# Optimization experiments

Measured on AMD Instinct MI355X. Metric: run time of the kernel, lower is better.

Reference implementation:

```python
import jax, jax.numpy as jnp
import numpy as np

B, N, D_IN, D, H = 4, 256, 600, 600, 256  # batch, nodes, in_dim, mem_dim, attn hidden


def setup_inputs() -> dict:
    key = jax.random.key(0)
    ks = jax.random.split(key, 12)
    feature = jax.random.normal(ks[0], (B, N, D_IN), dtype=jnp.float32)
    latent_adj = jax.random.randint(ks[1], (B, N, N), 0, 2).astype(jnp.float32)
    s_in = 1.0 / np.sqrt(D_IN)
    s_d = 1.0 / np.sqrt(D)
    s_2d = 1.0 / np.sqrt(2 * D)
    s_h = 1.0 / np.sqrt(H)
    W0 = jax.random.uniform(ks[2], (D_IN, D), jnp.float32, -s_in, s_in)
    b0 = jax.random.uniform(ks[3], (D,), jnp.float32, -s_in, s_in)
    W1 = jax.random.uniform(ks[4], (D, D), jnp.float32, -s_d, s_d)
    b1 = jax.random.uniform(ks[5], (D,), jnp.float32, -s_d, s_d)
    aW1 = jax.random.uniform(ks[6], (2 * D, H), jnp.float32, -s_2d, s_2d)
    ab1 = jax.random.uniform(ks[7], (H,), jnp.float32, -s_2d, s_2d)
    aW2 = jax.random.uniform(ks[8], (H,), jnp.float32, -s_h, s_h)
    ab2 = jax.random.uniform(ks[9], (1,), jnp.float32, -s_h, s_h)
    return {"feature": feature, "latent_adj": latent_adj, "W0": W0, "b0": b0,
            "W1": W1, "b1": b1, "aW1": aW1, "ab1": ab1, "aW2": aW2, "ab2": ab2}


def _gat_layer(x, Wl, bl, aW1, ab1, aW2, ab2, adj):
    h = jnp.einsum('bni,io->bno', x, Wl) + bl                    # [B,N,D]
    # Decompose first attn linear: [h_i, h_j] @ aW1 = h_i @ aW1[:D] + h_j @ aW1[D:]
    left = jnp.einsum('bnd,dh->bnh', h, aW1[:h.shape[-1]])        # i-part
    right = jnp.einsum('bnd,dh->bnh', h, aW1[h.shape[-1]:])       # j-part
    hid = jax.nn.relu(left[:, :, None, :] + right[:, None, :, :] + ab1)  # [B,N,N,H]
    e = jax.nn.leaky_relu(jnp.einsum('bijh,h->bij', hid, aW2) + ab2[0],
                          negative_slope=0.01)                    # [B,N,N]
    e = jnp.where(adj == 0, jnp.float32(-1e9), e)
    attention = jax.nn.softmax(e, axis=-1) * adj
    return jax.nn.relu(jnp.einsum('bij,bjd->bid', attention, h))


def reference(feature, latent_adj, W0, b0, W1, b1, aW1, ab1, aW2, ab2):
    h = _gat_layer(feature, W0, b0, aW1, ab1, aW2, ab2, latent_adj)
    h = _gat_layer(h, W1, b1, aW1, ab1, aW2, ab2, latent_adj)
    return h
```

## Files before the change

### kernel.cpp

```cpp
#include <hip/hip_runtime.h>
#include <hip/hip_bf16.h>

#define BATCH 4
#define NN    256
#define DD    600
#define HH    256
#define MROWS (BATCH*NN)
#define KPAD  640

typedef __attribute__((ext_vector_type(8))) short bf16x8;
typedef __attribute__((ext_vector_type(4))) float f32x4;

__device__ __forceinline__ void gload16(const void* g, void* l)
{
    __builtin_amdgcn_global_load_lds(
        (const __attribute__((address_space(1))) void*)g,
        (__attribute__((address_space(3))) void*)l, 16, 0, 0);
}

__device__ __forceinline__ void waitcnt_vm(int n)
{
    switch (n) {
    case 0:  asm volatile("s_waitcnt vmcnt(0)"  ::: "memory"); break;
    case 3:  asm volatile("s_waitcnt vmcnt(3)"  ::: "memory"); break;
    case 6:  asm volatile("s_waitcnt vmcnt(6)"  ::: "memory"); break;
    default: asm volatile("s_waitcnt vmcnt(0)"  ::: "memory"); break;
    }
}

__device__ __forceinline__ int xcd_remap(int lin, int nwg)
{
    const int q = nwg >> 3, r = nwg & 7;
    const int xcd = lin & 7, off = lin >> 3;
    return (xcd < r ? xcd * (q + 1) : r * (q + 1) + (xcd - r) * q) + off;
}

template<bool BIAS, bool RELU, bool WF32, bool WB16, bool WHT, int NK>
__global__ __launch_bounds__(256) void gemm_mfma(
    const __hip_bfloat16* __restrict__ A, const __hip_bfloat16* __restrict__ BT,
    const float* __restrict__ bias,
    float* __restrict__ Cf, __hip_bfloat16* __restrict__ Cb,
    __hip_bfloat16* __restrict__ hT,
    int lda, int ldb, int ldcf, int ldcb, int Nvalid, int biasN,
    long long sA, long long sBT, long long sCf, long long sCb)
{
    __shared__ __align__(16) char lds[49152];

    const int nwg = gridDim.x * gridDim.y * gridDim.z;
    int lin = xcd_remap(blockIdx.x + gridDim.x * (blockIdx.y + gridDim.y * blockIdx.z), nwg);
    const int bx = lin % gridDim.x;
    const int by = (lin / gridDim.x) % gridDim.y;
    const int bz = lin / (gridDim.x * gridDim.y);

    const int tid  = threadIdx.x;
    const int lane = tid & 63;
    const int wid  = tid >> 6;
    const int wr   = wid >> 1;
    const int wc   = wid & 1;
    const int row0 = by * 64;
    const int col0 = bx * 32;

    const char* Ab = (const char*)A + (bz * sA + (long long)row0 * lda) * 2;
    const char* Bb = (const char*)BT + (bz * sBT + (long long)col0 * ldb) * 2;

    const int sr   = tid >> 3;
    const int scb  = (tid & 7) * 16;
    const int scbs = scb ^ ((sr & 7) << 4);

    const char* gA0 = Ab + (long long)sr        * (lda * 2) + scbs;
    const char* gA1 = Ab + (long long)(sr + 32) * (lda * 2) + scbs;
    const char* gB0 = Bb + (long long)sr        * (ldb * 2) + scbs;

    f32x4 acc[2] = {};
    const int fr = lane & 15;
    const int kg = (lane >> 4) * 16;
    const int xv = (fr & 7) << 4;

    auto issue = [&](int t) {
        char* bA = lds + (t & 3) * 8192;
        char* bB = lds + 32768 + (t & 3) * 4096;
        const long long off = (long long)t * 128;
        gload16(gA0 + off, bA + wid * 1024);
        gload16(gA1 + off, bA + 4096 + wid * 1024);
        gload16(gB0 + off, bB + wid * 1024);
    };

    constexpr int PRE = (NK < 3) ? NK : 3;
    #pragma unroll
    for (int p = 0; p < PRE; ++p) issue(p);

    #pragma unroll
    for (int t = 0; t < NK; ++t) {
        const int imax = (t + 2 < NK - 1) ? t + 2 : NK - 1;
        waitcnt_vm(3 * (imax - t));
        __builtin_amdgcn_s_barrier();
        const char* lA = lds + (t & 3) * 8192;
        const char* lB = lds + 32768 + (t & 3) * 4096;
        #pragma unroll
        for (int ks = 0; ks < 2; ++ks) {
            const int kb = ks * 64 + kg;
            bf16x8 a0 = *(const bf16x8*)(lA + (wr * 32 + fr)      * 128 + (kb ^ xv));
            bf16x8 a1 = *(const bf16x8*)(lA + (wr * 32 + 16 + fr) * 128 + (kb ^ xv));
            bf16x8 b0 = *(const bf16x8*)(lB + (wc * 16 + fr)      * 128 + (kb ^ xv));
            acc[0] = __builtin_amdgcn_mfma_f32_16x16x32_bf16(a0, b0, acc[0], 0, 0, 0);
            acc[1] = __builtin_amdgcn_mfma_f32_16x16x32_bf16(a1, b0, acc[1], 0, 0, 0);
        }
        if (t + 3 < NK) issue(t + 3);
    }
    __syncthreads();

    const int er = (lane >> 4) * 4;
    const int ec = lane & 15;
    __hip_bfloat16* sT = (__hip_bfloat16*)lds;

    #pragma unroll
    for (int mi = 0; mi < 2; ++mi) {
        const int lr0 = wr * 32 + mi * 16 + er;
        const int lc  = wc * 16 + ec;
        const int gr = row0 + lr0;
        const int gc = col0 + lc;
        const float bv = (BIAS && gc < biasN) ? bias[gc] : 0.f;
        #pragma unroll
        for (int r = 0; r < 4; ++r) {
            float v = acc[mi][r] + bv;
            if (RELU) v = fmaxf(v, 0.f);
            const __hip_bfloat16 hv = __float2bfloat16(v);
            const long long row = gr + r;
            if (WF32 && gc < Nvalid)
                Cf[bz * sCf + row * ldcf + gc] = v;
            if (WB16)
                Cb[bz * sCb + row * ldcb + gc] = hv;
            if (WHT)
                sT[(lr0 + r) * 40 + lc] = hv;
        }
    }

    if (WHT) {
        __syncthreads();
        const int b  = row0 >> 8;
        const int i0 = row0 & 255;
        const int cc = tid >> 3;
        const int ch = tid & 7;
        const int d = col0 + cc;
        __align__(16) __hip_bfloat16 tmp[8];
        #pragma unroll
        for (int u = 0; u < 8; ++u)
            tmp[u] = sT[(ch * 8 + u) * 40 + cc];
        *(float4*)&hT[((long long)b * KPAD + d) * NN + i0 + ch * 8] = *(float4*)tmp;
    }
}

__global__ __launch_bounds__(256) void prep_kernel(
    const float* __restrict__ feature, const float* __restrict__ W0,
    const float* __restrict__ W1, const float* __restrict__ aW1,
    __hip_bfloat16* __restrict__ xb, __hip_bfloat16* __restrict__ W0T,
    __hip_bfloat16* __restrict__ W1T, __hip_bfloat16* __restrict__ aW1T)
{
    const int bid = blockIdx.x;
    const int tid = threadIdx.x;
    if (bid < 640) {
        const int idx = (bid * 256 + tid) * 4;
        const int r = idx / KPAD, c = idx % KPAD;
        float4 v = make_float4(0.f, 0.f, 0.f, 0.f);
        if (c < DD) v = *(const float4*)&feature[r * DD + c];
        __align__(8) __hip_bfloat16 o[4] = {
            __float2bfloat16(v.x), __float2bfloat16(v.y),
            __float2bfloat16(v.z), __float2bfloat16(v.w)};
        *(float2*)&xb[idx] = *(float2*)o;
        return;
    }
    __shared__ float tile[32][33];
    const int t = bid - 640;
    const int which = (t < 400) ? 0 : (t < 800) ? 1 : 2;
    const int tt = (which == 0) ? t : (which == 1) ? t - 400 : t - 800;
    const int n0 = (tt / 20) * 32;
    const int k0 = (tt % 20) * 32;
    const int tx = tid & 31, ty = tid >> 5;
    #pragma unroll
    for (int r = 0; r < 4; ++r) {
        const int k = k0 + ty + r * 8;
        const int n = n0 + tx;
        float v = 0.f;
        if (which == 0)      { if (k < DD && n < DD) v = W0[k * DD + n]; }
        else if (which == 1) { if (k < DD && n < DD) v = W1[k * DD + n]; }
        else                 { if (k < DD) v = (n < HH) ? aW1[k * HH + n]
                                                        : aW1[(DD + k) * HH + (n - HH)]; }
        tile[ty + r * 8][tx] = v;
    }
    __syncthreads();
    __hip_bfloat16* dst = (which == 0) ? W0T : (which == 1) ? W1T : aW1T;
    #pragma unroll
    for (int r = 0; r < 4; ++r) {
        const int n = n0 + ty + r * 8;
        const int k = k0 + tx;
        dst[n * KPAD + k] = __float2bfloat16(tile[tx][ty + r * 8]);
    }
}

__device__ __forceinline__ void block_max4(float* v, float (*red)[4])
{
    #pragma unroll
    for (int o = 32; o > 0; o >>= 1)
        #pragma unroll
        for (int q = 0; q < 4; ++q) v[q] = fmaxf(v[q], __shfl_down(v[q], o));
    const int lane = threadIdx.x & 63, w = threadIdx.x >> 6;
    if (lane == 0) { red[w][0]=v[0]; red[w][1]=v[1]; red[w][2]=v[2]; red[w][3]=v[3]; }
    __syncthreads();
    #pragma unroll
    for (int q = 0; q < 4; ++q)
        v[q] = fmaxf(fmaxf(red[0][q], red[1][q]), fmaxf(red[2][q], red[3][q]));
    __syncthreads();
}

__device__ __forceinline__ void block_sum4(float* v, float (*red)[4])
{
    #pragma unroll
    for (int o = 32; o > 0; o >>= 1)
        #pragma unroll
        for (int q = 0; q < 4; ++q) v[q] += __shfl_down(v[q], o);
    const int lane = threadIdx.x & 63, w = threadIdx.x >> 6;
    if (lane == 0) { red[w][0]=v[0]; red[w][1]=v[1]; red[w][2]=v[2]; red[w][3]=v[3]; }
    __syncthreads();
    #pragma unroll
    for (int q = 0; q < 4; ++q)
        v[q] = red[0][q] + red[1][q] + red[2][q] + red[3][q];
    __syncthreads();
}

__global__ __launch_bounds__(256) void attn_kernel(
    const float* __restrict__ LR, const float* __restrict__ aW2,
    const float* __restrict__ ab2, const float* __restrict__ adj,
    __hip_bfloat16* __restrict__ att)
{
    __shared__ float sL[4][HH];
    __shared__ float sW[HH];
    __shared__ float red[4][4];

    const int b  = blockIdx.y;
    const int i0 = blockIdx.x * 4;
    const int j  = threadIdx.x;

    float a[4];
    #pragma unroll
    for (int q = 0; q < 4; ++q)
        a[q] = adj[((long long)(b * NN + i0 + q)) * NN + j];
    const float ab2v = ab2[0];

    sW[j] = aW2[j];
    #pragma unroll
    for (int q = 0; q < 4; ++q)
        sL[q][j] = LR[((long long)(b * NN + i0 + q)) * 512 + j];
    __syncthreads();

    const float* rp = LR + ((long long)(b * NN + j)) * 512 + HH;
    float acc[4] = {0.f, 0.f, 0.f, 0.f};
    for (int h = 0; h < HH; h += 8) {
        const float4 ra = *(const float4*)(rp + h);
        const float4 rb = *(const float4*)(rp + h + 4);
        const float4 w0 = *(const float4*)&sW[h];
        const float4 w1 = *(const float4*)&sW[h + 4];
        #pragma unroll
        for (int q = 0; q < 4; ++q) {
            const float4 l0 = *(const float4*)&sL[q][h];
            const float4 l1 = *(const float4*)&sL[q][h + 4];
            float s = fmaxf(l0.x + ra.x, 0.f) * w0.x;
            s += fmaxf(l0.y + ra.y, 0.f) * w0.y;
            s += fmaxf(l0.z + ra.z, 0.f) * w0.z;
            s += fmaxf(l0.w + ra.w, 0.f) * w0.w;
            s += fmaxf(l1.x + rb.x, 0.f) * w1.x;
            s += fmaxf(l1.y + rb.y, 0.f) * w1.y;
            s += fmaxf(l1.z + rb.z, 0.f) * w1.z;
            s += fmaxf(l1.w + rb.w, 0.f) * w1.w;
            acc[q] += s;
        }
    }

    float m[4];
    #pragma unroll
    for (int q = 0; q < 4; ++q) {
        float e = acc[q] + ab2v;
        e = (e > 0.f) ? e : 0.01f * e;
        m[q] = (a[q] == 0.f) ? -1e9f : e;
    }
    float mx[4] = {m[0], m[1], m[2], m[3]};
    block_max4(mx, red);
    float p[4];
    #pragma unroll
    for (int q = 0; q < 4; ++q) p[q] = __expf(m[q] - mx[q]);
    float s[4] = {p[0], p[1], p[2], p[3]};
    block_sum4(s, red);
    #pragma unroll
    for (int q = 0; q < 4; ++q)
        att[((long long)(b * NN + i0 + q)) * NN + j] = __float2bfloat16(p[q] / s[q] * a[q]);
}

extern "C" void kernel_launch(void* const* d_in, const int* in_sizes, int n_in,
                              void* d_out, int out_size, void* d_ws, size_t ws_size,
                              hipStream_t stream)
{
    const float* feature = (const float*)d_in[0];
    const float* adj     = (const float*)d_in[1];
    const float* W0      = (const float*)d_in[2];
    const float* b0      = (const float*)d_in[3];
    const float* W1      = (const float*)d_in[4];
    const float* b1      = (const float*)d_in[5];
    const float* aW1     = (const float*)d_in[6];
    const float* ab1     = (const float*)d_in[7];
    const float* aW2     = (const float*)d_in[8];
    const float* ab2     = (const float*)d_in[9];
    float* out = (float*)d_out;

    __hip_bfloat16* bw = (__hip_bfloat16*)d_ws;
    __hip_bfloat16* xb   = bw;
    __hip_bfloat16* W0T  = xb   + MROWS * KPAD;
    __hip_bfloat16* W1T  = W0T  + KPAD * KPAD;
    __hip_bfloat16* aW1T = W1T  + KPAD * KPAD;
    __hip_bfloat16* hb   = aW1T + 512 * KPAD;
    __hip_bfloat16* hT   = hb   + MROWS * KPAD;
    __hip_bfloat16* att  = hT   + BATCH * KPAD * NN;
    float* LR = (float*)(att + BATCH * NN * NN);

    prep_kernel<<<1760, 256, 0, stream>>>(feature, W0, W1, aW1, xb, W0T, W1T, aW1T);

    for (int layer = 0; layer < 2; ++layer) {
        const __hip_bfloat16* WT = layer ? W1T : W0T;
        const float* bb          = layer ? b1 : b0;

        gemm_mfma<true, false, false, true, true, KPAD/64>
            <<<dim3(KPAD / 32, MROWS / 64, 1), 256, 0, stream>>>(
            xb, WT, bb, nullptr, hb, hT,
            KPAD, KPAD, 0, KPAD, 0, DD, 0, 0, 0, 0);

        gemm_mfma<true, false, true, false, false, KPAD/64>
            <<<dim3(512 / 32, MROWS / 64, 1), 256, 0, stream>>>(
            hb, aW1T, ab1, LR, nullptr, nullptr,
            KPAD, KPAD, 512, 0, 512, HH, 0, 0, 0, 0);

        attn_kernel<<<dim3(NN / 4, BATCH), 256, 0, stream>>>(LR, aW2, ab2, adj, att);

        if (layer == 0) {
            gemm_mfma<false, true, false, true, false, NN/64>
                <<<dim3(KPAD / 32, NN / 64, BATCH), 256, 0, stream>>>(
                att, hT, nullptr, nullptr, xb, nullptr,
                NN, NN, 0, KPAD, 0, 0,
                (long long)NN * NN, (long long)KPAD * NN, 0, (long long)NN * KPAD);
        } else {
            gemm_mfma<false, true, true, false, false, NN/64>
                <<<dim3(KPAD / 32, NN / 64, BATCH), 256, 0, stream>>>(
                att, hT, nullptr, out, nullptr, nullptr,
                NN, NN, DD, 0, DD, 0,
                (long long)NN * NN, (long long)KPAD * NN, (long long)NN * DD, 0);
        }
    }
}
```

Before: 64.61 us.

## Fuse attention softmax with attention-times-h GEMM in one kernel

Merges the attention-score/softmax kernel with the following attention@h batched GEMM. Each block now computes 4 attention rows, keeps them in LDS as bf16, and streams the full hT for its batch through a triple-buffered LDS pipeline into MFMA with relu applied in the epilogue. This removes one launch per layer and the global round trip of the attention matrix. In exchange, each block re-reads all of hT (256x640) for only 4 output rows. It also uses a 16-row MFMA tile where only 4 rows are valid, so most of the matrix-core work is wasted.

```diff
diff --git a/kernel.cpp b/kernel.cpp
--- a/kernel.cpp
+++ b/kernel.cpp
@@ -7,6 +7,7 @@
 #define HH    256
 #define MROWS (BATCH*NN)
 #define KPAD  640
+#define ATTS  272
 
 typedef __attribute__((ext_vector_type(8))) short bf16x8;
 typedef __attribute__((ext_vector_type(4))) float f32x4;
@@ -23,6 +24,7 @@
     switch (n) {
     case 0:  asm volatile("s_waitcnt vmcnt(0)"  ::: "memory"); break;
     case 3:  asm volatile("s_waitcnt vmcnt(3)"  ::: "memory"); break;
+    case 4:  asm volatile("s_waitcnt vmcnt(4)"  ::: "memory"); break;
     case 6:  asm volatile("s_waitcnt vmcnt(6)"  ::: "memory"); break;
     default: asm volatile("s_waitcnt vmcnt(0)"  ::: "memory"); break;
     }
@@ -35,22 +37,20 @@
     return (xcd < r ? xcd * (q + 1) : r * (q + 1) + (xcd - r) * q) + off;
 }
 
-template<bool BIAS, bool RELU, bool WF32, bool WB16, bool WHT, int NK>
+template<bool BIAS, bool WF32, bool WB16, bool WHT, int NK>
 __global__ __launch_bounds__(256) void gemm_mfma(
     const __hip_bfloat16* __restrict__ A, const __hip_bfloat16* __restrict__ BT,
     const float* __restrict__ bias,
     float* __restrict__ Cf, __hip_bfloat16* __restrict__ Cb,
     __hip_bfloat16* __restrict__ hT,
-    int lda, int ldb, int ldcf, int ldcb, int Nvalid, int biasN,
-    long long sA, long long sBT, long long sCf, long long sCb)
+    int lda, int ldb, int ldcf, int ldcb, int Nvalid, int biasN)
 {
     __shared__ __align__(16) char lds[49152];
 
-    const int nwg = gridDim.x * gridDim.y * gridDim.z;
-    int lin = xcd_remap(blockIdx.x + gridDim.x * (blockIdx.y + gridDim.y * blockIdx.z), nwg);
+    const int nwg = gridDim.x * gridDim.y;
+    int lin = xcd_remap(blockIdx.x + gridDim.x * blockIdx.y, nwg);
     const int bx = lin % gridDim.x;
-    const int by = (lin / gridDim.x) % gridDim.y;
-    const int bz = lin / (gridDim.x * gridDim.y);
+    const int by = lin / gridDim.x;
 
     const int tid  = threadIdx.x;
     const int lane = tid & 63;
@@ -60,8 +60,8 @@
     const int row0 = by * 64;
     const int col0 = bx * 32;
 
-    const char* Ab = (const char*)A + (bz * sA + (long long)row0 * lda) * 2;
-    const char* Bb = (const char*)BT + (bz * sBT + (long long)col0 * ldb) * 2;
+    const char* Ab = (const char*)A + ((long long)row0 * lda) * 2;
+    const char* Bb = (const char*)BT + ((long long)col0 * ldb) * 2;
 
     const int sr   = tid >> 3;
     const int scb  = (tid & 7) * 16;
@@ -123,13 +123,12 @@
         #pragma unroll
         for (int r = 0; r < 4; ++r) {
             float v = acc[mi][r] + bv;
-            if (RELU) v = fmaxf(v, 0.f);
             const __hip_bfloat16 hv = __float2bfloat16(v);
             const long long row = gr + r;
             if (WF32 && gc < Nvalid)
-                Cf[bz * sCf + row * ldcf + gc] = v;
+                Cf[row * ldcf + gc] = v;
             if (WB16)
-                Cb[bz * sCb + row * ldcb + gc] = hv;
+                Cb[row * ldcb + gc] = hv;
             if (WHT)
                 sT[(lr0 + r) * 40 + lc] = hv;
         }
@@ -227,18 +226,25 @@
     __syncthreads();
 }
 
-__global__ __launch_bounds__(256) void attn_kernel(
+template<bool OUTF32>
+__global__ __launch_bounds__(256) void attn_pv(
     const float* __restrict__ LR, const float* __restrict__ aW2,
     const float* __restrict__ ab2, const float* __restrict__ adj,
-    __hip_bfloat16* __restrict__ att)
-{
-    __shared__ float sL[4][HH];
-    __shared__ float sW[HH];
-    __shared__ float red[4][4];
+    const __hip_bfloat16* __restrict__ hT,
+    __hip_bfloat16* __restrict__ Ob, float* __restrict__ Of)
+{
+    __shared__ __align__(16) char smem[57344];
+    float (*sL)[HH] = (float(*)[HH])(smem + 49152);
+    float* sW       = (float*)(smem + 49152 + 4096);
+    float (*red)[4] = (float(*)[4])(smem + 49152 + 5120);
+    __hip_bfloat16* attl = (__hip_bfloat16*)(smem + 49152 + 5120 + 64);
 
     const int b  = blockIdx.y;
     const int i0 = blockIdx.x * 4;
     const int j  = threadIdx.x;
+    const int tid  = threadIdx.x;
+    const int lane = tid & 63;
+    const int wid  = tid >> 6;
 
     float a[4];
     #pragma unroll
@@ -253,7 +259,7 @@
     __syncthreads();
 
     const float* rp = LR + ((long long)(b * NN + j)) * 512 + HH;
-    float acc[4] = {0.f, 0.f, 0.f, 0.f};
+    float acs[4] = {0.f, 0.f, 0.f, 0.f};
     for (int h = 0; h < HH; h += 8) {
         const float4 ra = *(const float4*)(rp + h);
         const float4 rb = *(const float4*)(rp + h + 4);
@@ -271,14 +277,14 @@
             s += fmaxf(l1.y + rb.y, 0.f) * w1.y;
             s += fmaxf(l1.z + rb.z, 0.f) * w1.z;
             s += fmaxf(l1.w + rb.w, 0.f) * w1.w;
-            acc[q] += s;
+            acs[q] += s;
         }
     }
 
     float m[4];
     #pragma unroll
     for (int q = 0; q < 4; ++q) {
-        float e = acc[q] + ab2v;
+        float e = acs[q] + ab2v;
         e = (e > 0.f) ? e : 0.01f * e;
         m[q] = (a[q] == 0.f) ? -1e9f : e;
     }
@@ -287,11 +293,76 @@
     float p[4];
     #pragma unroll
     for (int q = 0; q < 4; ++q) p[q] = __expf(m[q] - mx[q]);
-    float s[4] = {p[0], p[1], p[2], p[3]};
-    block_sum4(s, red);
+    float s4[4] = {p[0], p[1], p[2], p[3]};
+    block_sum4(s4, red);
+
     #pragma unroll
     for (int q = 0; q < 4; ++q)
-        att[((long long)(b * NN + i0 + q)) * NN + j] = __float2bfloat16(p[q] / s[q] * a[q]);
+        attl[q * ATTS + j] = __float2bfloat16(p[q] / s4[q] * a[q]);
+
+    asm volatile("s_waitcnt lgkmcnt(0)" ::: "memory");
+    asm volatile("s_waitcnt vmcnt(0)" ::: "memory");
+    __builtin_amdgcn_s_barrier();
+
+    const char* hTb = (const char*)(hT + (long long)b * KPAD * NN);
+    const int rsub = wid * 4 + (lane >> 4);
+    const int cb16 = (lane & 15) * 16;
+
+    auto stage = [&](int c) {
+        char* buf = smem + (c % 3) * 16384;
+        const int d0 = (c >> 1) * 64;
+        const int ko = (c & 1) * 256;
+        #pragma unroll
+        for (int i = 0; i < 4; ++i) {
+            const int r = i * 16 + rsub;
+            gload16(hTb + (long long)(d0 + r) * 512 + ko + (cb16 ^ ((r & 7) << 4)),
+                    buf + i * 4096 + wid * 1024);
+        }
+    };
+
+    f32x4 acc[10] = {};
+    const int fr = lane & 15;
+    const int kg = (lane >> 4) * 16;
+    const int xv = (fr & 7) << 4;
+    const int arow = lane & 15;
+
+    stage(0); stage(1);
+    #pragma unroll
+    for (int c = 0; c < 20; ++c) {
+        waitcnt_vm(c < 19 ? 4 : 0);
+        __builtin_amdgcn_s_barrier();
+        const char* buf = smem + (c % 3) * 16384;
+        const int t  = c >> 1;
+        const int kt = c & 1;
+        #pragma unroll
+        for (int ks = 0; ks < 4; ++ks) {
+            const int kb = ks * 64 + kg;
+            bf16x8 bfr = *(const bf16x8*)(buf + (wid * 16 + fr) * 256 + (kb ^ xv));
+            bf16x8 afr = {};
+            if (arow < 4)
+                afr = *(const bf16x8*)((const char*)attl + arow * (ATTS * 2)
+                                       + (kt * 128 + ks * 32 + (lane >> 4) * 8) * 2);
+            acc[t] = __builtin_amdgcn_mfma_f32_16x16x32_bf16(afr, bfr, acc[t], 0, 0, 0);
+        }
+        if (c + 2 < 20) stage(c + 2);
+    }
+
+    if ((lane >> 4) == 0) {
+        #pragma unroll
+        for (int t = 0; t < 10; ++t) {
+            const int gc = t * 64 + wid * 16 + (lane & 15);
+            #pragma unroll
+            for (int r = 0; r < 4; ++r) {
+                const float v = fmaxf(acc[t][r], 0.f);
+                const long long row = (long long)(b * NN + i0 + r);
+                if (OUTF32) {
+                    if (gc < DD) Of[row * DD + gc] = v;
+                } else {
+                    Ob[row * KPAD + gc] = __float2bfloat16(v);
+                }
+            }
+        }
+    }
 }
 
 extern "C" void kernel_launch(void* const* d_in, const int* in_sizes, int n_in,
@@ -317,8 +388,7 @@
     __hip_bfloat16* aW1T = W1T  + KPAD * KPAD;
     __hip_bfloat16* hb   = aW1T + 512 * KPAD;
     __hip_bfloat16* hT   = hb   + MROWS * KPAD;
-    __hip_bfloat16* att  = hT   + BATCH * KPAD * NN;
-    float* LR = (float*)(att + BATCH * NN * NN);
+    float* LR = (float*)(hT + BATCH * KPAD * NN);
 
     prep_kernel<<<1760, 256, 0, stream>>>(feature, W0, W1, aW1, xb, W0T, W1T, aW1T);
 
@@ -326,30 +396,22 @@
         const __hip_bfloat16* WT = layer ? W1T : W0T;
         const float* bb          = layer ? b1 : b0;
 
-        gemm_mfma<true, false, false, true, true, KPAD/64>
-            <<<dim3(KPAD / 32, MROWS / 64, 1), 256, 0, stream>>>(
+        gemm_mfma<true, false, true, true, KPAD/64>
+            <<<dim3(KPAD / 32, MROWS / 64), 256, 0, stream>>>(
             xb, WT, bb, nullptr, hb, hT,
-            KPAD, KPAD, 0, KPAD, 0, DD, 0, 0, 0, 0);
-
-        gemm_mfma<true, false, true, false, false, KPAD/64>
-            <<<dim3(512 / 32, MROWS / 64, 1), 256, 0, stream>>>(
+            KPAD, KPAD, 0, KPAD, 0, DD);
+
+        gemm_mfma<true, true, false, false, KPAD/64>
+            <<<dim3(512 / 32, MROWS / 64), 256, 0, stream>>>(
             hb, aW1T, ab1, LR, nullptr, nullptr,
-            KPAD, KPAD, 512, 0, 512, HH, 0, 0, 0, 0);
-
-        attn_kernel<<<dim3(NN / 4, BATCH), 256, 0, stream>>>(LR, aW2, ab2, adj, att);
+            KPAD, KPAD, 512, 0, 512, HH);
 
         if (layer == 0) {
-            gemm_mfma<false, true, false, true, false, NN/64>
-                <<<dim3(KPAD / 32, NN / 64, BATCH), 256, 0, stream>>>(
-                att, hT, nullptr, nullptr, xb, nullptr,
-                NN, NN, 0, KPAD, 0, 0,
-                (long long)NN * NN, (long long)KPAD * NN, 0, (long long)NN * KPAD);
+            attn_pv<false><<<dim3(NN / 4, BATCH), 256, 0, stream>>>(
+                LR, aW2, ab2, adj, hT, xb, nullptr);
         } else {
-            gemm_mfma<false, true, true, false, false, NN/64>
-                <<<dim3(KPAD / 32, NN / 64, BATCH), 256, 0, stream>>>(
-                att, hT, nullptr, out, nullptr, nullptr,
-                NN, NN, DD, 0, DD, 0,
-                (long long)NN * NN, (long long)KPAD * NN, (long long)NN * DD, 0);
-        }
-    }
-}
+            attn_pv<true><<<dim3(NN / 4, BATCH), 256, 0, stream>>>(
+                LR, aW2, ab2, adj, hT, nullptr, out);
+        }
+    }
+}
```

Result: slower. 74.42 us (+15.2%).
